# Kernel optimization log

Hardware: AMD Instinct MI355X
Metric: run time of the kernel (lower is better)

The kernel has to match this reference:

```python
import jax, jax.numpy as jnp
import numpy as np

H = W = 1024          # image_shape (square)
ZP, PH, PW = 16, 32, 32   # psf z-stack shape
THRESH = 2.0          # detection_threshold
K = 1024              # spots_per_frame
ROISIZE = PW          # default roisize = psf.shape[-1]
BG_R = PW * 2         # default bg_filter_size
MAXF = PW             # default max_filter_size


def setup_inputs() -> dict:
    key = jax.random.key(0)
    k1, k2 = jax.random.split(key)
    image = jax.random.uniform(k1, (H, W), jnp.float32) * 100.0
    psf = jax.random.uniform(k2, (ZP, PH, PW), jnp.float32)
    psf = psf / jnp.sum(psf, axis=(1, 2), keepdims=True)  # normalized PSF stack
    return {"image": image, "psf": psf}


def _precompute_filters(psf):
    pad = (H - PH) // 2  # square image/psf -> same pad both dims
    psf_padded = jnp.pad(psf, ((0, 0), (pad, pad), (pad, pad)))
    psf_padded = jnp.fft.fftshift(psf_padded, axes=(1, 2))
    psf_fd = jnp.flip(jnp.fft.fft2(psf_padded), axis=(1, 2))
    rr = (jnp.arange(H) - H // 2)[:, None] ** 2 + (jnp.arange(W) - W // 2)[None, :] ** 2
    bg = (rr < BG_R ** 2).astype(jnp.float32) / (np.pi * BG_R ** 2)
    bg_fd = jnp.fft.fft2(jnp.fft.fftshift(bg))
    return psf_fd, bg_fd


def reference(image, psf):
    psf_fd, bg_fd = _precompute_filters(psf)
    image_fd = jnp.fft.fft2(image)
    conv_psf = jnp.fft.ifft2(image_fd[None] * psf_fd).real       # [Z,H,W]
    conv_bg = jnp.fft.ifft2(image_fd * bg_fd).real               # [H,W]
    ratio = conv_psf / (conv_bg[None] + 1.0)                     # matched-filter SNR
    result = ratio.max(axis=0)                                   # [H,W]
    zmap = jnp.argmax(ratio, axis=0)                             # best z plane

    # MaxPool2d(MAXF, stride=1, padding=MAXF//2-1): torch pads with -inf,
    # output is [H-1,W-1]; torch code then zero-pads one row/col at top-left.
    p = MAXF // 2 - 1
    mx = jax.lax.reduce_window(result, -jnp.inf, jax.lax.max,
                               (MAXF, MAXF), (1, 1), ((p, p), (p, p)))
    mx = jnp.pad(mx, ((1, 0), (1, 0)))                           # back to [H,W]

    mask = jnp.where((mx == result) & (result > THRESH), result, 0.0)
    values, indices = jax.lax.top_k(mask.ravel(), K)
    x = indices % W
    y = indices // H  # torch divides by input_shape[0]; square so == W
    roy = y - ROISIZE // 2
    rox = x - ROISIZE // 2
    valid = ((values > THRESH)
             & (roy >= 0) & (roy < H - ROISIZE)
             & (rox >= 0) & (rox < W - ROISIZE))

    # fixed-shape version of boolean select: clamp for safe gather, mask invalids
    roy_c = jnp.clip(roy, 0, H - ROISIZE)
    rox_c = jnp.clip(rox, 0, W - ROISIZE)
    r = jnp.arange(ROISIZE)
    Y = roy_c[:, None, None] + r[None, :, None]                  # [K,R,1]
    X = rox_c[:, None, None] + r[None, None, :]                  # [K,1,R]
    rois = image[Y, X] * valid[:, None, None].astype(image.dtype)  # [K,R,R]

    roipos = jnp.stack((roy_c, rox_c), -1) * valid[:, None]
    intensity = values * valid
    return roipos, intensity, rois, valid
```

## Files before the change

kernel.cpp:

```cpp
#include <hip/hip_runtime.h>
#include <stdint.h>

typedef float v4f __attribute__((ext_vector_type(4)));
typedef float f2u __attribute__((ext_vector_type(2), aligned(4)));

#define PEX_STRIDE 1156
#define CSTRIDE 858
#define WS_IMG8   0
#define WS_BFRAG  1048576
#define WS_PEX    1064960
#define WS_RB     5799936
#define WS_RESULT 9994240
#define WS_CAND   14188544

__device__ inline unsigned char f32_to_e4m3(float v) {
    if (!(v > 0.0f)) return 0;
    if (v >= 448.0f) return 0x7e;
    if (v < 0.015625f) {
        int m = (int)(v * 512.0f + 0.5f);
        if (m > 7) return 0x08;
        return (unsigned char)m;
    }
    unsigned int u = __float_as_uint(v) + 0x00080000u;
    int e = (int)((u >> 23) & 0xff) - 127;
    int m3 = (int)(u >> 20) & 7;
    int e8 = e + 7;
    if (e8 >= 16) return 0x7e;
    return (unsigned char)((e8 << 3) | m3);
}

__global__ void k_pex(const float* __restrict__ img, float* __restrict__ pex,
                      uint32_t* __restrict__ img8, const float* __restrict__ psf,
                      unsigned char* __restrict__ bf, unsigned int* cnt,
                      float4* __restrict__ out, int n4) {
    __shared__ float wtot[4];
    int blk = blockIdx.x, t = threadIdx.x;
    if (blk >= 1024) {
        if (blk < 2080) {
            int i = (blk - 1024) * 256 + t;
            if (i < n4) { float4 z; z.x = z.y = z.z = z.w = 0.f; out[i] = z; }
        } else {
            int u = (blk - 2080) * 256 + t;
            if (u == 0) { cnt[0] = 0u; cnt[2] = 0u; }
            int kb = u >> 9; int l = (u >> 3) & 63; int j = u & 7;
            int z = l & 15; int q = l >> 4;
            int a = kb; int b = q * 8 + j;
            float p = psf[z * 1024 + a * 32 + b];
            float c = cosf((float)(a + b - 32) * (6.283185307179586f / 1024.0f));
            bf[kb * 512 + l * 8 + j] = f32_to_e4m3(p * c * 1024.0f);
        }
        return;
    }
    int r = blk;
    const float* row = img + r * 1024;
    float s[5];
    float acc = 0.f;
    int base = t * 5;
    #pragma unroll
    for (int j = 0; j < 5; j++) {
        int c = base + j;
        float v = (c < 1152) ? row[(c - 64) & 1023] : 0.f;
        acc += v; s[j] = acc;
    }
    float sc = acc;
    int lane = t & 63, w = t >> 6;
    #pragma unroll
    for (int off = 1; off < 64; off <<= 1) {
        float v = __shfl_up(sc, off, 64);
        if (lane >= off) sc += v;
    }
    if (lane == 63) wtot[w] = sc;
    __syncthreads();
    float wbase = 0.f;
    #pragma unroll
    for (int i = 0; i < 3; i++) if (i < w) wbase += wtot[i];
    float excl = wbase + (sc - acc);
    float* prow = pex + r * PEX_STRIDE;
    if (t == 0) prow[0] = 0.f;
    #pragma unroll
    for (int j = 0; j < 5; j++) {
        int c = base + j;
        if (c < 1152) prow[c + 1] = excl + s[j];
    }
    float4 v4 = *(const float4*)(row + 4 * t);
    img8[r * 256 + t] = (uint32_t)f32_to_e4m3(v4.x)
                      | ((uint32_t)f32_to_e4m3(v4.y) << 8)
                      | ((uint32_t)f32_to_e4m3(v4.z) << 16)
                      | ((uint32_t)f32_to_e4m3(v4.w) << 24);
}

__global__ __launch_bounds__(256) void k_bg(const float* __restrict__ pex,
                                            float* __restrict__ rb) {
    static constexpr int W[64] = {
        63,63,63,63,63,63,63,63,63,63,63,63,
        62,62,62,62, 61,61,61,61, 60,60,60, 59,59, 58,58,58, 57,57, 56,
        55,55, 54,54, 53, 52,52, 51, 50, 49,49,
        48,47,46,45,44,43,42,41,
        39,38,37,35,34,32,30,29,27,24,22,19,15,11
    };
    int blk = blockIdx.x;
    int xcd = blk & 7;
    int sub = blk >> 4;
    int half = (blk >> 3) & 1;
    int s = xcd * 8 + sub;
    int row = s * 16 + 7;
    int n0 = (half << 9) + ((int)threadIdx.x << 1);
    f2u acc0, acc1;
    {
        const float* pr = pex + row * PEX_STRIDE + n0;
        acc0 = *(const f2u*)(pr + 128) - *(const f2u*)(pr + 1);
        acc1 = (f2u)0.f;
    }
    #pragma unroll 3
    for (int dy = 1; dy <= 63; dy++) {
        const int w = W[dy];
        const float* p1 = pex + ((row - dy) & 1023) * PEX_STRIDE + n0;
        const float* p2 = pex + ((row + dy) & 1023) * PEX_STRIDE + n0;
        acc0 += *(const f2u*)(p1 + 65 + w) - *(const f2u*)(p1 + 64 - w);
        acc1 += *(const f2u*)(p2 + 65 + w) - *(const f2u*)(p2 + 64 - w);
    }
    f2u sum = acc0 + acc1;
    const float k = (float)(1.0 / (3.14159265358979323846 * 4096.0));
    f2u r2;
    r2.x = 1.0f / ((sum.x * k + 1.0f) * 1024.0f);
    r2.y = 1.0f / ((sum.y * k + 1.0f) * 1024.0f);
    *(f2u*)(rb + s * 1024 + n0) = r2;
}

__global__ __launch_bounds__(512, 2) void k_conv(
    const unsigned long long* __restrict__ img64,
    const unsigned long long* __restrict__ bfrag,
    const float* __restrict__ rb, float* __restrict__ result,
    float* __restrict__ tilemax) {
    __shared__ unsigned long long sm[8 * CSTRIDE];
    __shared__ float bmax[8];
    int tid = threadIdx.x;
    int wave = tid >> 6, lane = tid & 63;
    int b = blockIdx.x;
    int tr = b >> 5, tc = b & 31;
    int r0 = tr * 64, c0 = tc * 32;

    for (int u = tid; u < 665; u += 512) {
        int dr = u / 7;
        int x8 = u - dr * 7;
        int row = (r0 + dr - 16) & 1023;
        int cb0 = (c0 + x8 * 8 - 16) & 1023;
        int cb1 = (cb0 + 8) & 1023;
        unsigned long long lo = img64[row * 128 + (cb0 >> 3)];
        unsigned long long hi = img64[row * 128 + (cb1 >> 3)];
        int dst = dr * 9 + x8;
        sm[dst] = lo;
        #pragma unroll
        for (int s = 1; s < 8; s++)
            sm[s * CSTRIDE + dst] = (lo >> (8 * s)) | (hi << (64 - 8 * s));
    }
    __syncthreads();

    int i0 = (wave >> 1) * 16;
    int cw = (wave & 1) * 16;
    int g = lane >> 4;
    int slot = ((cw + (lane & 15)) >> 3) + g;
    const unsigned long long* bp = sm + (lane & 7) * CSTRIDE + slot + i0 * 9;

    unsigned long long breg[16];
    #pragma unroll
    for (int j = 0; j < 16; j++) breg[j] = bp[j * 9];

    v4f acc[16];
    #pragma unroll
    for (int f = 0; f < 16; f++) acc[f] = (v4f)0.0f;

    unsigned long long anext = bfrag[lane];
    #pragma unroll
    for (int kb = 0; kb < 32; kb++) {
        unsigned long long acur = anext;
        anext = bfrag[((kb < 31 ? kb + 1 : 31) << 6) + lane];
        #pragma unroll
        for (int cc = 0; cc < 16; cc++) {
            acc[cc] = __builtin_amdgcn_mfma_f32_16x16x32_fp8_fp8(
                (long)acur, (long)breg[(kb + cc) & 15], acc[cc], 0, 0, 0);
        }
        breg[kb & 15] = bp[(kb < 31 ? kb + 16 : 46) * 9];
    }

    float zmax[16];
    float wm = -3.4e38f;
    #pragma unroll
    for (int cc = 0; cc < 16; cc++) {
        v4f v = acc[cc];
        float m = fmaxf(fmaxf(v.x, v.y), fmaxf(v.z, v.w));
        m = fmaxf(m, __shfl_xor(m, 16, 64));
        m = fmaxf(m, __shfl_xor(m, 32, 64));
        zmax[cc] = m;
        wm = fmaxf(wm, m);
    }
    int gcol = c0 + cw + (lane & 15);
    #pragma unroll
    for (int c4 = 0; c4 < 4; c4++) {
        float m01 = (g & 1) ? zmax[c4 * 4 + 1] : zmax[c4 * 4 + 0];
        float m23 = (g & 1) ? zmax[c4 * 4 + 3] : zmax[c4 * 4 + 2];
        float m = (g & 2) ? m23 : m01;
        int grow = r0 + i0 + c4 * 4 + g;
        result[grow * 1024 + gcol] = m * rb[(grow >> 4) * 1024 + gcol];
    }
    float pm = -3.4e38f;
    #pragma unroll
    for (int c4 = 0; c4 < 4; c4++) {
        float m01 = (g & 1) ? zmax[c4 * 4 + 1] : zmax[c4 * 4 + 0];
        float m23 = (g & 1) ? zmax[c4 * 4 + 3] : zmax[c4 * 4 + 2];
        float m = (g & 2) ? m23 : m01;
        int grow = r0 + i0 + c4 * 4 + g;
        pm = fmaxf(pm, m * rb[(grow >> 4) * 1024 + gcol]);
    }
    #pragma unroll
    for (int d = 1; d < 64; d <<= 1) pm = fmaxf(pm, __shfl_xor(pm, d, 64));
    if (lane == 0) bmax[wave] = pm;
    __syncthreads();
    if (tid == 0) {
        float m = bmax[0];
        #pragma unroll
        for (int i = 1; i < 8; i++) m = fmaxf(m, bmax[i]);
        tilemax[b] = m;
    }
}

__global__ __launch_bounds__(256) void k_maxcand(
    const float* __restrict__ result, const float* __restrict__ tilemax,
    unsigned int* cnt, unsigned long long* cand,
    const float* __restrict__ image, float* __restrict__ out) {
    __shared__ __align__(16) char smbuf[61184];
    __shared__ float wmaxdummy;  (void)wmaxdummy;
    __shared__ unsigned int lastv;
    float* ls = (float*)smbuf;
    float* hr = (float*)(smbuf + 36480);
    unsigned long long* keys = (unsigned long long*)smbuf;
    int b = blockIdx.x;
    int bx = b & 15, by = b >> 4;
    int i0 = by * 64, j0 = bx * 64;
    int t = threadIdx.x;
    unsigned int* done = cnt + 2;

    float tm = fmaxf(tilemax[by * 32 + 2 * bx], tilemax[by * 32 + 2 * bx + 1]);
    if (tm > 2.0f) {
        for (int idx = t; idx < 95 * 95; idx += 256) {
            int r = idx / 95, c = idx - r * 95;
            int gr = i0 - 16 + r, gc = j0 - 16 + c;
            float v = -3.4e38f;
            if ((unsigned)gr < 1024u && (unsigned)gc < 1024u) v = result[gr * 1024 + gc];
            ls[r * 96 + c] = v;
        }
        __syncthreads();
        for (int idx = t; idx < 95 * 64; idx += 256) {
            int r = idx >> 6, c = idx & 63;
            const float* p = ls + r * 96 + c;
            float m = p[0];
            #pragma unroll
            for (int d = 1; d < 32; d++) m = fmaxf(m, p[d]);
            hr[idx] = m;
        }
        __syncthreads();
        for (int idx = t; idx < 64 * 64; idx += 256) {
            int r = idx >> 6, c = idx & 63;
            const float* p = hr + r * 64 + c;
            float m = p[0];
            #pragma unroll
            for (int d = 1; d < 32; d++) m = fmaxf(m, p[d * 64]);
            float v = ls[(r + 16) * 96 + (c + 16)];
            int gi = i0 + r, gj = j0 + c;
            if (gi >= 1 && gj >= 1 && v > 2.0f && v == m) {
                unsigned int k = atomicAdd(cnt, 1u);
                if (k < 2048)
                    cand[k] = ((unsigned long long)__float_as_uint(v) << 32)
                            | (unsigned int)(~(unsigned int)(gi * 1024 + gj));
            }
        }
        __syncthreads();
    }

    __threadfence();
    if (t == 0) lastv = atomicAdd(done, 1u);
    __syncthreads();
    if (lastv != 255) return;
    __threadfence();

    int n = (int)cnt[0]; if (n > 2048) n = 2048;
    if (n == 0) return;
    for (int k = t; k < 2048; k += 256) keys[k] = (k < n) ? cand[k] : 0ull;
    __syncthreads();
    for (int size = 2; size <= 2048; size <<= 1) {
        for (int stride = size >> 1; stride > 0; stride >>= 1) {
            for (int i = t; i < 2048; i += 256) {
                int ixj = i ^ stride;
                if (ixj > i) {
                    unsigned long long a = keys[i], bb = keys[ixj];
                    bool sw = ((i & size) == 0) ? (a < bb) : (a > bb);
                    if (sw) { keys[i] = bb; keys[ixj] = a; }
                }
            }
            __syncthreads();
        }
    }
    float* roipos = out;
    float* intensity = out + 2048;
    float* rois = out + 3072;
    float* validf = out + 3072 + 1048576;
    int nw = n < 1024 ? n : 1024;
    for (int k = t; k < nw; k += 256) {
        unsigned long long key = keys[k];
        float val = __uint_as_float((unsigned int)(key >> 32));
        unsigned int p = ~(unsigned int)key;
        int y = (int)(p >> 10), x = (int)(p & 1023);
        int roy = y - 16, rox = x - 16;
        bool valid = (roy >= 0 && roy < 992 && rox >= 0 && rox < 992);
        int royc = roy < 0 ? 0 : (roy > 992 ? 992 : roy);
        int roxc = rox < 0 ? 0 : (rox > 992 ? 992 : rox);
        roipos[2 * k]     = valid ? (float)royc : 0.f;
        roipos[2 * k + 1] = valid ? (float)roxc : 0.f;
        intensity[k]      = valid ? val : 0.f;
        validf[k]         = valid ? 1.f : 0.f;
    }
    __syncthreads();
    for (int k = 0; k < nw; k++) {
        unsigned long long key = keys[k];
        unsigned int p = ~(unsigned int)key;
        int y = (int)(p >> 10), x = (int)(p & 1023);
        int roy = y - 16, rox = x - 16;
        if (!(roy >= 0 && roy < 992 && rox >= 0 && rox < 992)) continue;
        #pragma unroll
        for (int part = 0; part < 4; part++) {
            int tt = part * 256 + t;
            int u = tt >> 5, vv = tt & 31;
            rois[k * 1024 + tt] = image[(roy + u) * 1024 + (rox + vv)];
        }
    }
}

extern "C" void kernel_launch(void* const* d_in, const int* in_sizes, int n_in,
                              void* d_out, int out_size, void* d_ws, size_t ws_size,
                              hipStream_t stream) {
    const float* image = (const float*)d_in[0];
    const float* psf   = (const float*)d_in[1];
    float* out = (float*)d_out;
    char* ws = (char*)d_ws;
    unsigned char* img8  = (unsigned char*)(ws + WS_IMG8);
    unsigned char* bfrag = (unsigned char*)(ws + WS_BFRAG);
    float* pex = (float*)(ws + WS_PEX);
    float* rb  = (float*)(ws + WS_RB);
    float* result = (float*)(ws + WS_RESULT);
    unsigned int* cnt = (unsigned int*)(ws + WS_CAND);
    float* tilemax = (float*)(ws + WS_CAND + 1024);
    unsigned long long* cand = (unsigned long long*)(ws + WS_CAND + 4096);

    int n4 = out_size / 4;
    hipLaunchKernelGGL(k_pex,     dim3(2144), dim3(256), 0, stream,
                       image, pex, (uint32_t*)img8, psf, bfrag, cnt, (float4*)d_out, n4);
    hipLaunchKernelGGL(k_bg,      dim3(128),  dim3(256), 0, stream, pex, rb);
    hipLaunchKernelGGL(k_conv,    dim3(512),  dim3(512), 0, stream,
                       (const unsigned long long*)img8, (const unsigned long long*)bfrag,
                       rb, result, tilemax);
    hipLaunchKernelGGL(k_maxcand, dim3(256),  dim3(256), 0, stream,
                       result, tilemax, cnt, cand, image, out);
}
```

Measured before the change: 116.1 us.

## Split conv MFMA loop into two row halves to raise occupancy

The fp8 MFMA convolution loop in k_conv now processes the 16 output rows in two passes of 8 rather than one pass of 16. This halves the live accumulator and B-register arrays, and launch bounds are raised from 2 to 4 blocks per CU to trade registers for occupancy. In exchange the A-fragment stream from global memory is read twice per wave, and each pass has a shorter MFMA chain. The duplicated epilogue pass is also merged so result store and max reduction share one loop.

Measured after the change: 124.0 us. 1.07x slower.

```diff
diff --git a/kernel.cpp b/kernel.cpp
--- a/kernel.cpp
+++ b/kernel.cpp
@@ -127,7 +127,7 @@
     *(f2u*)(rb + s * 1024 + n0) = r2;
 }
 
-__global__ __launch_bounds__(512, 2) void k_conv(
+__global__ __launch_bounds__(512, 4) void k_conv(
     const unsigned long long* __restrict__ img64,
     const unsigned long long* __restrict__ bfrag,
     const float* __restrict__ rb, float* __restrict__ result,
@@ -161,57 +161,54 @@
     int g = lane >> 4;
     int slot = ((cw + (lane & 15)) >> 3) + g;
     const unsigned long long* bp = sm + (lane & 7) * CSTRIDE + slot + i0 * 9;
-
-    unsigned long long breg[16];
-    #pragma unroll
-    for (int j = 0; j < 16; j++) breg[j] = bp[j * 9];
-
-    v4f acc[16];
-    #pragma unroll
-    for (int f = 0; f < 16; f++) acc[f] = (v4f)0.0f;
-
-    unsigned long long anext = bfrag[lane];
-    #pragma unroll
-    for (int kb = 0; kb < 32; kb++) {
-        unsigned long long acur = anext;
-        anext = bfrag[((kb < 31 ? kb + 1 : 31) << 6) + lane];
-        #pragma unroll
-        for (int cc = 0; cc < 16; cc++) {
-            acc[cc] = __builtin_amdgcn_mfma_f32_16x16x32_fp8_fp8(
-                (long)acur, (long)breg[(kb + cc) & 15], acc[cc], 0, 0, 0);
-        }
-        breg[kb & 15] = bp[(kb < 31 ? kb + 16 : 46) * 9];
-    }
-
-    float zmax[16];
-    float wm = -3.4e38f;
-    #pragma unroll
-    for (int cc = 0; cc < 16; cc++) {
-        v4f v = acc[cc];
-        float m = fmaxf(fmaxf(v.x, v.y), fmaxf(v.z, v.w));
-        m = fmaxf(m, __shfl_xor(m, 16, 64));
-        m = fmaxf(m, __shfl_xor(m, 32, 64));
-        zmax[cc] = m;
-        wm = fmaxf(wm, m);
-    }
     int gcol = c0 + cw + (lane & 15);
-    #pragma unroll
-    for (int c4 = 0; c4 < 4; c4++) {
-        float m01 = (g & 1) ? zmax[c4 * 4 + 1] : zmax[c4 * 4 + 0];
-        float m23 = (g & 1) ? zmax[c4 * 4 + 3] : zmax[c4 * 4 + 2];
-        float m = (g & 2) ? m23 : m01;
-        int grow = r0 + i0 + c4 * 4 + g;
-        result[grow * 1024 + gcol] = m * rb[(grow >> 4) * 1024 + gcol];
-    }
     float pm = -3.4e38f;
-    #pragma unroll
-    for (int c4 = 0; c4 < 4; c4++) {
-        float m01 = (g & 1) ? zmax[c4 * 4 + 1] : zmax[c4 * 4 + 0];
-        float m23 = (g & 1) ? zmax[c4 * 4 + 3] : zmax[c4 * 4 + 2];
-        float m = (g & 2) ? m23 : m01;
-        int grow = r0 + i0 + c4 * 4 + g;
-        pm = fmaxf(pm, m * rb[(grow >> 4) * 1024 + gcol]);
-    }
+
+    #pragma unroll
+    for (int h = 0; h < 2; h++) {
+        const unsigned long long* bph = bp + h * 72;
+        unsigned long long breg[8];
+        #pragma unroll
+        for (int j = 0; j < 8; j++) breg[j] = bph[j * 9];
+        v4f acc[8];
+        #pragma unroll
+        for (int f = 0; f < 8; f++) acc[f] = (v4f)0.0f;
+
+        unsigned long long anext = bfrag[lane];
+        #pragma unroll
+        for (int kb = 0; kb < 32; kb++) {
+            unsigned long long acur = anext;
+            anext = bfrag[((kb < 31 ? kb + 1 : 31) << 6) + lane];
+            #pragma unroll
+            for (int j = 0; j < 8; j++) {
+                acc[j] = __builtin_amdgcn_mfma_f32_16x16x32_fp8_fp8(
+                    (long)acur, (long)breg[(kb + j) & 7], acc[j], 0, 0, 0);
+            }
+            int srel = (h == 0) ? (kb + 8) : (kb < 31 ? kb + 8 : 38);
+            breg[kb & 7] = bph[srel * 9];
+        }
+
+        float zx[8];
+        #pragma unroll
+        for (int j = 0; j < 8; j++) {
+            v4f v = acc[j];
+            float m = fmaxf(fmaxf(v.x, v.y), fmaxf(v.z, v.w));
+            m = fmaxf(m, __shfl_xor(m, 16, 64));
+            m = fmaxf(m, __shfl_xor(m, 32, 64));
+            zx[j] = m;
+        }
+        #pragma unroll
+        for (int c2 = 0; c2 < 2; c2++) {
+            float m01 = (g & 1) ? zx[c2 * 4 + 1] : zx[c2 * 4 + 0];
+            float m23 = (g & 1) ? zx[c2 * 4 + 3] : zx[c2 * 4 + 2];
+            float m = (g & 2) ? m23 : m01;
+            int grow = r0 + i0 + h * 8 + c2 * 4 + g;
+            float val = m * rb[(grow >> 4) * 1024 + gcol];
+            result[grow * 1024 + gcol] = val;
+            pm = fmaxf(pm, val);
+        }
+    }
+
     #pragma unroll
     for (int d = 1; d < 64; d <<= 1) pm = fmaxf(pm, __shfl_xor(pm, d, 64));
     if (lane == 0) bmax[wave] = pm;
@@ -229,7 +226,6 @@
     unsigned int* cnt, unsigned long long* cand,
     const float* __restrict__ image, float* __restrict__ out) {
     __shared__ __align__(16) char smbuf[61184];
-    __shared__ float wmaxdummy;  (void)wmaxdummy;
     __shared__ unsigned int lastv;
     float* ls = (float*)smbuf;
     float* hr = (float*)(smbuf + 36480);
```
